# Kernel optimization log

Measured on AMD Instinct MI355X. Metric: run time of the kernel, lower is better.

## Reference

```python
import jax, jax.numpy as jnp
import numpy as np

LN_EPS = 1e-5


def setup_inputs() -> dict:
    key = jax.random.key(0)
    ks = jax.random.split(key, 8)
    b, c, h, w = 16, 1024, 64, 64
    r = 64  # max(c // 16, 16)
    return {
        "x": jax.random.normal(ks[0], (b, c, h, w), dtype=jnp.float32),
        "wm": jax.random.normal(ks[1], (c,), dtype=jnp.float32) * 0.02,
        "bm": jax.random.normal(ks[2], (1,), dtype=jnp.float32) * 0.02,
        "w1": jax.random.normal(ks[3], (r, c), dtype=jnp.float32) * 0.02,
        "b1": jax.random.normal(ks[4], (r,), dtype=jnp.float32) * 0.02,
        "ln_g": jnp.ones((r,), dtype=jnp.float32),
        "ln_b": jnp.zeros((r,), dtype=jnp.float32),
        "w2": jax.random.normal(ks[5], (c, r), dtype=jnp.float32) * 0.02,
        "b2": jax.random.normal(ks[6], (c,), dtype=jnp.float32) * 0.02,
    }


def reference(x, wm, bm, w1, b1, ln_g, ln_b, w2, b2):
    b, c, h, w = x.shape
    s = h * w
    xf = x.reshape(b, c, s)  # [b, c, hw]
    # 1x1 conv mask: Conv2d(c -> 1)
    cm = jnp.einsum("bcs,c->bs", xf, wm) + bm  # [b, hw]
    unary = jax.nn.softmax(cm, axis=-1)  # softmax over spatial dim (dim=2 of [b,1,hw])
    # 'spatial' whitening: subtract mean over dim 1 (size 1) -> identically zero mask
    cm_w = cm - cm  # faithful to context_mask -= context_mask.mean(1).unsqueeze(1)
    mask = jax.nn.softmax(cm_w, axis=-1) + unary  # uniform 1/hw + unary
    # pooling: matmul(input_x [b,1,c,hw], mask [b,1,hw,1]) -> [b, c]
    context = jnp.einsum("bcs,bs->bc", xf, mask)
    # transform MLP: 1x1 conv -> LayerNorm([r,1,1]) -> ReLU -> 1x1 conv
    t = context @ w1.T + b1  # [b, r]
    mu = jnp.mean(t, axis=-1, keepdims=True)
    var = jnp.mean(jnp.square(t - mu), axis=-1, keepdims=True)
    t = (t - mu) * jax.lax.rsqrt(var + LN_EPS) * ln_g + ln_b
    t = jax.nn.relu(t)
    out = t @ w2.T + b2  # [b, c]
    return out.reshape(b, c, 1, 1)
```

## Files before the change

kernel.cpp:

```cpp
#include <hip/hip_runtime.h>
#include <hip/hip_bf16.h>

#define B 16
#define C 1024
#define S 4096
#define R 64
#define NCCHUNK 16
#define NSCHUNK 4

__global__ __launch_bounds__(256) void k1_cm_partial(
    const float* __restrict__ x, const float* __restrict__ wm,
    float* __restrict__ cm_part) {
  int bid = blockIdx.x;
  int cchunk = bid & (NCCHUNK - 1);
  int schunk = (bid >> 4) & (NSCHUNK - 1);
  int b = bid >> 6;
  int s0 = schunk * 1024 + threadIdx.x * 4;
  const float* xp = x + ((size_t)b * C + (size_t)cchunk * 64) * S + s0;
  const float* wp = wm + cchunk * 64;
  float4 acc = {0.f, 0.f, 0.f, 0.f};
#pragma unroll 4
  for (int c = 0; c < 64; ++c) {
    float w = wp[c];
    float4 v = *(const float4*)(xp + (size_t)c * S);
    acc.x += w * v.x; acc.y += w * v.y; acc.z += w * v.z; acc.w += w * v.w;
  }
  *(float4*)(cm_part + ((size_t)cchunk * B + b) * S + s0) = acc;
}

__global__ __launch_bounds__(256) void k2_softmax(
    const float* __restrict__ cm_part, float* __restrict__ e,
    float* __restrict__ zinv) {
  int b = blockIdx.x;
  float v[16];
#pragma unroll
  for (int j = 0; j < 16; ++j) {
    int s = threadIdx.x + j * 256;
    float acc = 0.f;
#pragma unroll
    for (int k = 0; k < NCCHUNK; ++k)
      acc += cm_part[((size_t)k * B + b) * S + s];
    v[j] = acc;
  }
  float m = -1e30f;
#pragma unroll
  for (int j = 0; j < 16; ++j) m = fmaxf(m, v[j]);
  for (int off = 32; off > 0; off >>= 1) m = fmaxf(m, __shfl_xor(m, off));
  __shared__ float redm[4], redz[4];
  int wid = threadIdx.x >> 6, lane = threadIdx.x & 63;
  if (lane == 0) redm[wid] = m;
  __syncthreads();
  m = fmaxf(fmaxf(redm[0], redm[1]), fmaxf(redm[2], redm[3]));
  float zs = 0.f, ev[16];
#pragma unroll
  for (int j = 0; j < 16; ++j) { ev[j] = expf(v[j] - m); zs += ev[j]; }
  for (int off = 32; off > 0; off >>= 1) zs += __shfl_xor(zs, off);
  if (lane == 0) redz[wid] = zs;
  __syncthreads();
  zs = redz[0] + redz[1] + redz[2] + redz[3];
#pragma unroll
  for (int j = 0; j < 16; ++j)
    e[(size_t)b * S + threadIdx.x + j * 256] = ev[j];
  if (threadIdx.x == 0) zinv[b] = 1.0f / zs;
}

__global__ __launch_bounds__(256) void k3_context(
    const float* __restrict__ x, const float* __restrict__ e,
    const float* __restrict__ zinv, float* __restrict__ context) {
  int row = blockIdx.x * 4 + (threadIdx.x >> 6);
  int lane = threadIdx.x & 63;
  int b = row >> 10;
  const float* xp = x + (size_t)row * S;
  const float* ep = e + (size_t)b * S;
  float s1 = 0.f, s2 = 0.f;
#pragma unroll
  for (int i = 0; i < 16; ++i) {
    int idx = lane * 4 + i * 256;
    float4 xv = *(const float4*)(xp + idx);
    float4 evv = *(const float4*)(ep + idx);
    s1 += xv.x + xv.y + xv.z + xv.w;
    s2 += xv.x * evv.x + xv.y * evv.y + xv.z * evv.z + xv.w * evv.w;
  }
  for (int off = 32; off > 0; off >>= 1) {
    s1 += __shfl_down(s1, off);
    s2 += __shfl_down(s2, off);
  }
  if (lane == 0) context[row] = s1 * (1.0f / S) + s2 * zinv[b];
}

__global__ __launch_bounds__(256) void k4_mlp(
    const float* __restrict__ context, const float* __restrict__ w1,
    const float* __restrict__ b1, const float* __restrict__ ln_g,
    const float* __restrict__ ln_b, const float* __restrict__ w2,
    const float* __restrict__ b2, float* __restrict__ out) {
  int b = blockIdx.x;
  __shared__ float ctx[C];
  __shared__ float tt[R];
  for (int j = threadIdx.x; j < C; j += 256) ctx[j] = context[b * C + j];
  __syncthreads();
  int r = threadIdx.x >> 2, q = threadIdx.x & 3;
  const float* w1p = w1 + (size_t)r * C + q * 256;
  const float* cp = ctx + q * 256;
  float part = 0.f;
#pragma unroll 4
  for (int i = 0; i < 256; ++i) part += cp[i] * w1p[i];
  part += __shfl_down(part, 1);
  part += __shfl_down(part, 2);
  if (q == 0) tt[r] = part + b1[r];
  __syncthreads();
  if (threadIdx.x < 64) {
    float v = tt[threadIdx.x];
    float mu = v;
    for (int off = 1; off < 64; off <<= 1) mu += __shfl_xor(mu, off);
    mu *= (1.0f / R);
    float d = v - mu;
    float var = d * d;
    for (int off = 1; off < 64; off <<= 1) var += __shfl_xor(var, off);
    var *= (1.0f / R);
    float t = d * rsqrtf(var + 1e-5f) * ln_g[threadIdx.x] + ln_b[threadIdx.x];
    tt[threadIdx.x] = fmaxf(t, 0.0f);
  }
  __syncthreads();
  for (int c = threadIdx.x; c < C; c += 256) {
    float acc = b2[c];
    const float* w2p = w2 + (size_t)c * R;
#pragma unroll
    for (int r2 = 0; r2 < R; ++r2) acc += tt[r2] * w2p[r2];
    out[b * C + c] = acc;
  }
}

extern "C" void kernel_launch(void* const* d_in, const int* in_sizes, int n_in,
                              void* d_out, int out_size, void* d_ws, size_t ws_size,
                              hipStream_t stream) {
  const float* x    = (const float*)d_in[0];
  const float* wm   = (const float*)d_in[1];
  const float* w1   = (const float*)d_in[3];
  const float* b1   = (const float*)d_in[4];
  const float* ln_g = (const float*)d_in[5];
  const float* ln_b = (const float*)d_in[6];
  const float* w2   = (const float*)d_in[7];
  const float* b2   = (const float*)d_in[8];
  float* out = (float*)d_out;

  float* ws = (float*)d_ws;
  float* cm_part = ws;
  float* e       = cm_part + (size_t)NCCHUNK * B * S;
  float* zinv    = e + (size_t)B * S;
  float* context = zinv + 64;

  k1_cm_partial<<<B * NSCHUNK * NCCHUNK, 256, 0, stream>>>(x, wm, cm_part);
  k2_softmax<<<B, 256, 0, stream>>>(cm_part, e, zinv);
  k3_context<<<B * C / 4, 256, 0, stream>>>(x, e, zinv, context);
  k4_mlp<<<B, 256, 0, stream>>>(context, w1, b1, ln_g, ln_b, w2, b2, out);
}
```

Before: 434.0 us.

## Vectorize all four kernels with ext_vector float4 and nontemporal loads of x

New measurement: 417.2 us. 1.04x faster.

```diff
diff --git a/kernel.cpp b/kernel.cpp
--- a/kernel.cpp
+++ b/kernel.cpp
@@ -8,6 +8,8 @@
 #define NCCHUNK 16
 #define NSCHUNK 4
 
+typedef float f4 __attribute__((ext_vector_type(4)));
+
 __global__ __launch_bounds__(256) void k1_cm_partial(
     const float* __restrict__ x, const float* __restrict__ wm,
     float* __restrict__ cm_part) {
@@ -15,53 +17,60 @@
   int cchunk = bid & (NCCHUNK - 1);
   int schunk = (bid >> 4) & (NSCHUNK - 1);
   int b = bid >> 6;
-  int s0 = schunk * 1024 + threadIdx.x * 4;
-  const float* xp = x + ((size_t)b * C + (size_t)cchunk * 64) * S + s0;
+  int s0 = schunk * 256 + threadIdx.x;
+  const f4* xp = (const f4*)x + ((size_t)b * C + (size_t)cchunk * 64) * (S / 4) + s0;
   const float* wp = wm + cchunk * 64;
-  float4 acc = {0.f, 0.f, 0.f, 0.f};
-#pragma unroll 4
-  for (int c = 0; c < 64; ++c) {
-    float w = wp[c];
-    float4 v = *(const float4*)(xp + (size_t)c * S);
-    acc.x += w * v.x; acc.y += w * v.y; acc.z += w * v.z; acc.w += w * v.w;
+  f4 a0 = {0.f, 0.f, 0.f, 0.f}, a1 = {0.f, 0.f, 0.f, 0.f};
+#pragma unroll 8
+  for (int c = 0; c < 64; c += 2) {
+    f4 v0 = __builtin_nontemporal_load(xp + (size_t)c * (S / 4));
+    f4 v1 = __builtin_nontemporal_load(xp + (size_t)(c + 1) * (S / 4));
+    a0 += wp[c] * v0;
+    a1 += wp[c + 1] * v1;
   }
-  *(float4*)(cm_part + ((size_t)cchunk * B + b) * S + s0) = acc;
+  ((f4*)cm_part)[((size_t)cchunk * B + b) * (S / 4) + s0] = a0 + a1;
 }
 
 __global__ __launch_bounds__(256) void k2_softmax(
     const float* __restrict__ cm_part, float* __restrict__ e,
     float* __restrict__ zinv) {
-  int b = blockIdx.x;
-  float v[16];
+  int b = blockIdx.x, tid = threadIdx.x;
+  f4 v[4] = {{0.f,0.f,0.f,0.f},{0.f,0.f,0.f,0.f},{0.f,0.f,0.f,0.f},{0.f,0.f,0.f,0.f}};
 #pragma unroll
-  for (int j = 0; j < 16; ++j) {
-    int s = threadIdx.x + j * 256;
-    float acc = 0.f;
+  for (int k = 0; k < NCCHUNK; ++k) {
+    const f4* cp = (const f4*)cm_part + ((size_t)k * B + b) * (S / 4);
 #pragma unroll
-    for (int k = 0; k < NCCHUNK; ++k)
-      acc += cm_part[((size_t)k * B + b) * S + s];
-    v[j] = acc;
+    for (int j = 0; j < 4; ++j) v[j] += cp[tid + j * 256];
   }
   float m = -1e30f;
 #pragma unroll
-  for (int j = 0; j < 16; ++j) m = fmaxf(m, v[j]);
+  for (int j = 0; j < 4; ++j)
+    m = fmaxf(m, fmaxf(fmaxf(v[j][0], v[j][1]), fmaxf(v[j][2], v[j][3])));
   for (int off = 32; off > 0; off >>= 1) m = fmaxf(m, __shfl_xor(m, off));
   __shared__ float redm[4], redz[4];
-  int wid = threadIdx.x >> 6, lane = threadIdx.x & 63;
+  int wid = tid >> 6, lane = tid & 63;
   if (lane == 0) redm[wid] = m;
   __syncthreads();
   m = fmaxf(fmaxf(redm[0], redm[1]), fmaxf(redm[2], redm[3]));
-  float zs = 0.f, ev[16];
+  float zs = 0.f;
+  f4 ev[4];
 #pragma unroll
-  for (int j = 0; j < 16; ++j) { ev[j] = expf(v[j] - m); zs += ev[j]; }
+  for (int j = 0; j < 4; ++j) {
+#pragma unroll
+    for (int q = 0; q < 4; ++q) {
+      float t = expf(v[j][q] - m);
+      ev[j][q] = t;
+      zs += t;
+    }
+  }
   for (int off = 32; off > 0; off >>= 1) zs += __shfl_xor(zs, off);
   if (lane == 0) redz[wid] = zs;
   __syncthreads();
   zs = redz[0] + redz[1] + redz[2] + redz[3];
+  f4* ep = (f4*)(e + (size_t)b * S);
 #pragma unroll
-  for (int j = 0; j < 16; ++j)
-    e[(size_t)b * S + threadIdx.x + j * 256] = ev[j];
-  if (threadIdx.x == 0) zinv[b] = 1.0f / zs;
+  for (int j = 0; j < 4; ++j) ep[tid + j * 256] = ev[j];
+  if (tid == 0) zinv[b] = 1.0f / zs;
 }
 
 __global__ __launch_bounds__(256) void k3_context(
@@ -70,22 +79,21 @@
   int row = blockIdx.x * 4 + (threadIdx.x >> 6);
   int lane = threadIdx.x & 63;
   int b = row >> 10;
-  const float* xp = x + (size_t)row * S;
-  const float* ep = e + (size_t)b * S;
-  float s1 = 0.f, s2 = 0.f;
+  const f4* xp = (const f4*)(x + (size_t)row * S);
+  const f4* ep = (const f4*)(e + (size_t)b * S);
+  float zi = zinv[b];
+  f4 s1 = {0.f, 0.f, 0.f, 0.f}, s2 = {0.f, 0.f, 0.f, 0.f};
 #pragma unroll
   for (int i = 0; i < 16; ++i) {
-    int idx = lane * 4 + i * 256;
-    float4 xv = *(const float4*)(xp + idx);
-    float4 evv = *(const float4*)(ep + idx);
-    s1 += xv.x + xv.y + xv.z + xv.w;
-    s2 += xv.x * evv.x + xv.y * evv.y + xv.z * evv.z + xv.w * evv.w;
+    f4 xv = __builtin_nontemporal_load(xp + lane + i * 64);
+    f4 evv = ep[lane + i * 64];
+    s1 += xv;
+    s2 += xv * evv;
   }
-  for (int off = 32; off > 0; off >>= 1) {
-    s1 += __shfl_down(s1, off);
-    s2 += __shfl_down(s2, off);
-  }
-  if (lane == 0) context[row] = s1 * (1.0f / S) + s2 * zinv[b];
+  float tot = (s1[0] + s1[1] + s1[2] + s1[3]) * (1.0f / S) +
+              (s2[0] + s2[1] + s2[2] + s2[3]) * zi;
+  for (int off = 32; off > 0; off >>= 1) tot += __shfl_down(tot, off);
+  if (lane == 0) context[row] = tot;
 }
 
 __global__ __launch_bounds__(256) void k4_mlp(
@@ -94,22 +102,23 @@
     const float* __restrict__ ln_b, const float* __restrict__ w2,
     const float* __restrict__ b2, float* __restrict__ out) {
   int b = blockIdx.x;
-  __shared__ float ctx[C];
+  int tid = threadIdx.x, wid = tid >> 6, lane = tid & 63;
   __shared__ float tt[R];
-  for (int j = threadIdx.x; j < C; j += 256) ctx[j] = context[b * C + j];
+  const f4* ctxp = (const f4*)(context + (size_t)b * C);
+  f4 c0 = ctxp[lane], c1 = ctxp[lane + 64], c2 = ctxp[lane + 128], c3 = ctxp[lane + 192];
+#pragma unroll
+  for (int i = 0; i < 16; ++i) {
+    int r = wid * 16 + i;
+    const f4* wp = (const f4*)(w1 + (size_t)r * C);
+    f4 p = c0 * wp[lane] + c1 * wp[lane + 64] + c2 * wp[lane + 128] + c3 * wp[lane + 192];
+    float dot = p[0] + p[1] + p[2] + p[3];
+#pragma unroll
+    for (int off = 32; off > 0; off >>= 1) dot += __shfl_xor(dot, off);
+    if (lane == 0) tt[r] = dot + b1[r];
+  }
   __syncthreads();
-  int r = threadIdx.x >> 2, q = threadIdx.x & 3;
-  const float* w1p = w1 + (size_t)r * C + q * 256;
-  const float* cp = ctx + q * 256;
-  float part = 0.f;
-#pragma unroll 4
-  for (int i = 0; i < 256; ++i) part += cp[i] * w1p[i];
-  part += __shfl_down(part, 1);
-  part += __shfl_down(part, 2);
-  if (q == 0) tt[r] = part + b1[r];
-  __syncthreads();
-  if (threadIdx.x < 64) {
-    float v = tt[threadIdx.x];
+  if (tid < 64) {
+    float v = tt[tid];
     float mu = v;
     for (int off = 1; off < 64; off <<= 1) mu += __shfl_xor(mu, off);
     mu *= (1.0f / R);
@@ -117,16 +126,20 @@
     float var = d * d;
     for (int off = 1; off < 64; off <<= 1) var += __shfl_xor(var, off);
     var *= (1.0f / R);
-    float t = d * rsqrtf(var + 1e-5f) * ln_g[threadIdx.x] + ln_b[threadIdx.x];
-    tt[threadIdx.x] = fmaxf(t, 0.0f);
+    tt[tid] = fmaxf(d * rsqrtf(var + 1e-5f) * ln_g[tid] + ln_b[tid], 0.0f);
   }
   __syncthreads();
-  for (int c = threadIdx.x; c < C; c += 256) {
-    float acc = b2[c];
-    const float* w2p = w2 + (size_t)c * R;
+  f4 t4[16];
 #pragma unroll
-    for (int r2 = 0; r2 < R; ++r2) acc += tt[r2] * w2p[r2];
-    out[b * C + c] = acc;
+  for (int k = 0; k < 16; ++k) t4[k] = *(const f4*)(tt + k * 4);
+#pragma unroll
+  for (int cc = 0; cc < 4; ++cc) {
+    int c = tid + cc * 256;
+    const f4* w2p = (const f4*)(w2 + (size_t)c * R);
+    f4 acc = {0.f, 0.f, 0.f, 0.f};
+#pragma unroll
+    for (int k = 0; k < 16; ++k) acc += w2p[k] * t4[k];
+    out[(size_t)b * C + c] = acc[0] + acc[1] + acc[2] + acc[3] + b2[c];
   }
 }
 
```
